# Kernel tuning notes

Hardware: AMD Instinct MI355X
Metric: run time of the kernel (lower is better)

## Reference

```python
import jax, jax.numpy as jnp
import numpy as np

N, D, K_FRAC = 4096, 256, 0.5
EPS = 1e-5  # BatchNorm1d default eps


def setup_inputs() -> dict:
    key = jax.random.key(0)
    kg, kh, kw = jax.random.split(key, 3)
    # sparse binary adjacency with self-loops so all degrees > 0 (pow(D,-1) finite)
    g = (jax.random.uniform(kg, (N, N)) < 0.004).astype(jnp.float32)
    g = jnp.maximum(g, jnp.eye(N, dtype=jnp.float32))
    h = jax.random.normal(kh, (N, D), dtype=jnp.float32)
    return {
        "g": g,
        "h": h,
        "gamma": jnp.ones((D,), jnp.float32),
        "beta": jnp.zeros((D,), jnp.float32),
        "w_proj": jax.random.normal(kw, (D, 1), dtype=jnp.float32) / np.sqrt(D),
        "b_proj": jnp.zeros((1,), jnp.float32),
        "sigma1": jnp.array([0.2], jnp.float32),
    }


def reference(g, h, gamma, beta, w_proj, b_proj, sigma1):
    # BatchNorm1d in training mode: batch statistics over the node axis
    mu = h.mean(0)
    var = h.var(0)  # biased variance, as torch uses for normalization
    h = (h - mu) / jnp.sqrt(var + EPS) * gamma + beta

    deg = g.sum(1)                               # [N] == Z2
    agg = (g @ h) / deg[:, None]                 # diag(D^-1) @ (g @ h), no NxN diag materialized
    Z1 = jnp.abs(h - agg).sum(1)                 # [N]
    pl = jax.nn.sigmoid(Z1 + deg)
    Z3 = (agg @ w_proj + b_proj)[:, 0]           # proj(Z3).squeeze()
    pg = jax.nn.softmax(Z3)                      # 1-D softmax (dim 0)
    pt = jax.nn.sigmoid(pl + pg)
    pf = jax.nn.sigmoid((h @ w_proj + b_proj)[:, 0])
    scores = sigma1[0] * pt + (1.0 - sigma1[0]) * pf

    # top_k_graph
    k = max(2, int(K_FRAC * N))
    _, idx = jax.lax.top_k(scores, k)            # [k]
    h_att = scores[:, None] * h                  # score-weighted features
    un_g = (g != 0).astype(jnp.float32)
    two_hop = ((un_g @ un_g) != 0).astype(jnp.float32)  # binarized 2-hop adjacency
    a_hat = two_hop[idx, :]                      # [k, N] row gather
    new_h = a_hat @ h_att                        # [k, D]
    g_new = a_hat[:, idx]                        # [k, k] column gather
    # norm_g: torch broadcast divides COLUMN j by row-sum degrees[j]
    g_new = g_new / g_new.sum(1)
    return g_new, new_h, idx
```

## Files before the change

### kernel.cpp

```cpp
#include <hip/hip_runtime.h>
#include <math.h>

#define NN 4096
#define DD 256
#define KK 2048
#define NW 64

__global__ void k_stats_part(const float* __restrict__ h, double* __restrict__ psum,
                             double* __restrict__ psq) {
    int d = threadIdx.x;
    int b = blockIdx.x;
    int r0 = b * 64;
    double s0=0,s1=0,s2=0,s3=0,q0=0,q1=0,q2=0,q3=0;
    for (int k = 0; k < 64; k += 4) {
        double x0 = (double)h[(size_t)(r0+k+0) * DD + d];
        double x1 = (double)h[(size_t)(r0+k+1) * DD + d];
        double x2 = (double)h[(size_t)(r0+k+2) * DD + d];
        double x3 = (double)h[(size_t)(r0+k+3) * DD + d];
        s0 += x0; q0 += x0*x0;
        s1 += x1; q1 += x1*x1;
        s2 += x2; q2 += x2*x2;
        s3 += x3; q3 += x3*x3;
    }
    psum[b * DD + d] = (s0+s1)+(s2+s3);
    psq [b * DD + d] = (q0+q1)+(q2+q3);
}

__global__ void k_stats_final(const double* __restrict__ psum, const double* __restrict__ psq,
                              double* __restrict__ mu, double* __restrict__ rstd) {
    __shared__ double rs[4][DD];
    __shared__ double rq[4][DD];
    int t = threadIdx.x;
    int d = t & (DD - 1);
    int q = t >> 8;
    double s0=0,s1=0,q0=0,q1=0;
    int b0 = q * 16;
    for (int k = 0; k < 16; k += 2) {
        s0 += psum[(b0+k)   * DD + d];
        s1 += psum[(b0+k+1) * DD + d];
        q0 += psq [(b0+k)   * DD + d];
        q1 += psq [(b0+k+1) * DD + d];
    }
    rs[q][d] = s0 + s1;
    rq[q][d] = q0 + q1;
    __syncthreads();
    if (q == 0) {
        double S  = (rs[0][d]+rs[1][d]) + (rs[2][d]+rs[3][d]);
        double Q  = (rq[0][d]+rq[1][d]) + (rq[2][d]+rq[3][d]);
        double m  = S / (double)NN;
        double var = Q / (double)NN - m * m;
        mu[d]   = m;
        rstd[d] = 1.0 / sqrt(var + 1e-5);
    }
}

__global__ void k_norm_zpf(const float* __restrict__ h, const double* __restrict__ mu,
                           const double* __restrict__ rstd, const float* __restrict__ gamma,
                           const float* __restrict__ beta, const float* __restrict__ w,
                           const float* __restrict__ bp, float* __restrict__ hn,
                           double* __restrict__ zpf) {
    __shared__ double red[DD];
    int r = blockIdx.x;
    int d = threadIdx.x;
    size_t i = (size_t)r * DD + d;
    double hnd = ((double)h[i] - mu[d]) * rstd[d] * (double)gamma[d] + (double)beta[d];
    hn[i] = (float)hnd;
    red[d] = hnd * (double)w[d];
    __syncthreads();
    for (int s = 128; s > 0; s >>= 1) {
        if (d < s) red[d] += red[d + s];
        __syncthreads();
    }
    if (d == 0) zpf[r] = red[0] + (double)bp[0];
}

__global__ void k_bitmask(const float* __restrict__ g, unsigned long long* __restrict__ B) {
    int i = blockIdx.x;
    int t = threadIdx.x;
    int q = t >> 6, l = t & 63;
    const float4* g4 = (const float4*)(g + (size_t)i * NN);
    for (int wi = 0; wi < 4; ++wi) {
        float4 v = g4[q * 256 + wi * 64 + l];
        unsigned int nib = (unsigned int)(v.x != 0.f)
                         | ((unsigned int)(v.y != 0.f) << 1)
                         | ((unsigned int)(v.z != 0.f) << 2)
                         | ((unsigned int)(v.w != 0.f) << 3);
        unsigned long long word = (unsigned long long)nib << (4 * (l & 15));
        unsigned int lo = (unsigned int)word, hi = (unsigned int)(word >> 32);
        for (int s = 1; s < 16; s <<= 1) {
            lo |= __shfl_xor(lo, s, 16);
            hi |= __shfl_xor(hi, s, 16);
        }
        if ((l & 15) == 0)
            B[(size_t)i * NW + 16 * q + 4 * wi + (l >> 4)] =
                ((unsigned long long)hi << 32) | lo;
    }
}

__global__ void k_twohop(const unsigned long long* __restrict__ B,
                         unsigned long long* __restrict__ T) {
    int i = blockIdx.x;
    int t = threadIdx.x;
    int w = t >> 6, l = t & 63;
    __shared__ int cols[128];
    __shared__ int s_cnt;
    __shared__ unsigned long long red[4][NW];
    if (t < 64) {
        unsigned long long word = B[(size_t)i * NW + t];
        int pc = __popcll(word);
        int off = pc;
        for (int dlt = 1; dlt < 64; dlt <<= 1) {
            int n = __shfl_up(off, dlt);
            if (t >= dlt) off += n;
        }
        if (t == 63) s_cnt = off;
        int base = off - pc;
        while (word) {
            int b = (int)__ffsll(word) - 1;
            word &= word - 1;
            if (base < 128) cols[base] = t * 64 + b;
            ++base;
        }
    }
    __syncthreads();
    int cnt = s_cnt;
    unsigned long long a0 = 0ull, a1 = 0ull;
    int j = w;
    for (; j + 4 < cnt; j += 8) {
        a0 |= B[(size_t)cols[j]     * NW + l];
        a1 |= B[(size_t)cols[j + 4] * NW + l];
    }
    for (; j < cnt; j += 4) a0 |= B[(size_t)cols[j] * NW + l];
    red[w][l] = a0 | a1;
    __syncthreads();
    if (t < NW)
        T[(size_t)i * NW + t] = (red[0][t] | red[1][t]) | (red[2][t] | red[3][t]);
}

__global__ void k_agg(const float* __restrict__ h, const double* __restrict__ mu,
                      const double* __restrict__ rstd, const float* __restrict__ gamma,
                      const float* __restrict__ beta, const unsigned long long* __restrict__ B,
                      const float* __restrict__ w, const float* __restrict__ bp,
                      double* __restrict__ Z1, double* __restrict__ Z3,
                      int* __restrict__ degi) {
    int i = blockIdx.x;
    int t = threadIdx.x;
    int wv = t >> 6, l = t & 63;
    __shared__ int cols[128];
    __shared__ int s_cnt;
    __shared__ double redd[4][DD];
    __shared__ double red[DD];
    __shared__ double red2[DD];
    if (t < 64) {
        unsigned long long word = B[(size_t)i * NW + t];
        int pc = __popcll(word);
        int off = pc;
        for (int dlt = 1; dlt < 64; dlt <<= 1) {
            int n = __shfl_up(off, dlt);
            if (t >= dlt) off += n;
        }
        if (t == 63) s_cnt = off;
        int base = off - pc;
        while (word) {
            int b = (int)__ffsll(word) - 1;
            word &= word - 1;
            if (base < 128) cols[base] = t * 64 + b;
            ++base;
        }
    }
    __syncthreads();
    int cnt = s_cnt;
    if (t == 0) degi[i] = cnt;
    const float4* h4 = (const float4*)h;
    double a0=0,a1=0,a2=0,a3=0,b0=0,b1=0,b2=0,b3=0;
    int j = wv;
    for (; j + 4 < cnt; j += 8) {
        float4 v0 = h4[(size_t)cols[j]     * 64 + l];
        float4 v1 = h4[(size_t)cols[j + 4] * 64 + l];
        a0 += (double)v0.x; a1 += (double)v0.y; a2 += (double)v0.z; a3 += (double)v0.w;
        b0 += (double)v1.x; b1 += (double)v1.y; b2 += (double)v1.z; b3 += (double)v1.w;
    }
    for (; j < cnt; j += 4) {
        float4 v0 = h4[(size_t)cols[j] * 64 + l];
        a0 += (double)v0.x; a1 += (double)v0.y; a2 += (double)v0.z; a3 += (double)v0.w;
    }
    redd[wv][4*l+0] = a0 + b0;
    redd[wv][4*l+1] = a1 + b1;
    redd[wv][4*l+2] = a2 + b2;
    redd[wv][4*l+3] = a3 + b3;
    __syncthreads();
    double S = (redd[0][t] + redd[1][t]) + (redd[2][t] + redd[3][t]);
    double mud = mu[t], rsd = rstd[t];
    double aggd = (S / (double)cnt - mud) * rsd * (double)gamma[t] + (double)beta[t];
    double hni  = ((double)h[(size_t)i * DD + t] - mud) * rsd * (double)gamma[t] + (double)beta[t];
    red[t]  = fabs(hni - aggd);
    red2[t] = aggd * (double)w[t];
    __syncthreads();
    for (int s = 128; s > 0; s >>= 1) {
        if (t < s) { red[t] += red[t + s]; red2[t] += red2[t + s]; }
        __syncthreads();
    }
    if (t == 0) { Z1[i] = red[0]; Z3[i] = red2[0] + (double)bp[0]; }
}

__global__ void k_red1(const double* __restrict__ Z3, double* __restrict__ pm,
                       double* __restrict__ ps, unsigned long long* __restrict__ S) {
    __shared__ double sm[128];
    __shared__ double ss[128];
    int t = threadIdx.x;
    int b = blockIdx.x;
    if (b == 0 && t < NW) S[t] = 0ull;
    double z = Z3[b * 128 + t];
    sm[t] = z;
    __syncthreads();
    for (int s = 64; s > 0; s >>= 1) {
        if (t < s) sm[t] = fmax(sm[t], sm[t + s]);
        __syncthreads();
    }
    double m = sm[0];
    ss[t] = exp(z - m);
    __syncthreads();
    for (int s = 64; s > 0; s >>= 1) {
        if (t < s) ss[t] += ss[t + s];
        __syncthreads();
    }
    if (t == 0) { pm[b] = m; ps[b] = ss[0]; }
}

__global__ void k_scorekeys(const double* __restrict__ Z1, const double* __restrict__ Z3,
                            const double* __restrict__ zpf, const int* __restrict__ degi,
                            const float* __restrict__ sigma1, const double* __restrict__ pm,
                            const double* __restrict__ ps, float* __restrict__ scores,
                            unsigned long long* __restrict__ keys) {
    int i = blockIdx.x * 256 + threadIdx.x;
    double M = -1e300;
    for (int b = 0; b < 32; ++b) M = fmax(M, pm[b]);
    double sum = 0.0;
    for (int b = 0; b < 32; ++b) sum += ps[b] * exp(pm[b] - M);
    double s1 = (double)sigma1[0];
    double pg = exp(Z3[i] - M) / sum;
    double pl = 1.0 / (1.0 + exp(-(Z1[i] + (double)degi[i])));
    double pt = 1.0 / (1.0 + exp(-(pl + pg)));
    double pf = 1.0 / (1.0 + exp(-zpf[i]));
    float sc = (float)(s1 * pt + (1.0 - s1) * pf);
    scores[i] = sc;
    unsigned int b2 = __float_as_uint(sc);
    unsigned int ka = (b2 & 0x80000000u) ? ~b2 : (b2 ^ 0x80000000u);
    keys[i] = ((unsigned long long)(~ka) << 32) | (unsigned int)i;
}

__global__ void k_rank(const unsigned long long* __restrict__ keys, int* __restrict__ idx_int,
                       unsigned long long* __restrict__ S, float* __restrict__ out_idx) {
    __shared__ unsigned long long Kl[NN];
    int t = threadIdx.x;
    for (int i = t; i < NN; i += 256) Kl[i] = keys[i];
    __syncthreads();
    int il = t >> 4, sub = t & 15;
    int i = blockIdx.x * 16 + il;
    unsigned long long ki = Kl[i];
    int c0 = 0, c1 = 0, c2 = 0, c3 = 0;
    for (int jj = 0; jj < 256; jj += 4) {
        int j = sub + (jj << 4);
        c0 += (Kl[j]      < ki) ? 1 : 0;
        c1 += (Kl[j + 16] < ki) ? 1 : 0;
        c2 += (Kl[j + 32] < ki) ? 1 : 0;
        c3 += (Kl[j + 48] < ki) ? 1 : 0;
    }
    int cnt = (c0 + c1) + (c2 + c3);
    for (int off = 8; off > 0; off >>= 1) cnt += __shfl_down(cnt, off, 16);
    if (sub == 0) {
        int rank = cnt;
        if (rank < KK) {
            idx_int[rank] = i;
            out_idx[rank] = (float)i;
            atomicOr(&S[i >> 6], 1ull << (i & 63));
        }
    }
}

__global__ void k_rowsum(const unsigned long long* __restrict__ T, const int* __restrict__ idx_int,
                         const unsigned long long* __restrict__ S, float* __restrict__ inv_rs) {
    int j = blockIdx.x * 256 + threadIdx.x;
    if (j >= KK) return;
    int r = idx_int[j];
    int c = 0;
    for (int w = 0; w < NW; ++w) c += __popcll(T[(size_t)r * NW + w] & S[w]);
    inv_rs[j] = 1.0f / (float)c;
}

__global__ void k_gnew(const unsigned long long* __restrict__ T, const int* __restrict__ idx_int,
                       const float* __restrict__ inv_rs, float* __restrict__ out) {
    int r = blockIdx.x;
    int t = threadIdx.x;
    __shared__ unsigned long long Tl[NW];
    if (t < NW) Tl[t] = T[(size_t)idx_int[r] * NW + t];
    __syncthreads();
    const int4*   idx4 = (const int4*)idx_int;
    const float4* irs4 = (const float4*)inv_rs;
    float4* out4 = (float4*)(out + (size_t)r * KK);
    for (int c4 = t; c4 < KK / 4; c4 += 256) {
        int4 jc = idx4[c4];
        float4 iv = irs4[c4];
        float4 o;
        o.x = ((Tl[jc.x >> 6] >> (jc.x & 63)) & 1ull) ? iv.x : 0.0f;
        o.y = ((Tl[jc.y >> 6] >> (jc.y & 63)) & 1ull) ? iv.y : 0.0f;
        o.z = ((Tl[jc.z >> 6] >> (jc.z & 63)) & 1ull) ? iv.z : 0.0f;
        o.w = ((Tl[jc.w >> 6] >> (jc.w & 63)) & 1ull) ? iv.w : 0.0f;
        out4[c4] = o;
    }
}

__global__ void k_newh(const unsigned long long* __restrict__ T, const int* __restrict__ idx_int,
                       const float* __restrict__ scores, const float* __restrict__ hn,
                       float* __restrict__ out) {
    int r = blockIdx.x;
    int t = threadIdx.x;
    int wv = t >> 6, l = t & 63;
    __shared__ int cols[2048];
    __shared__ int s_cnt;
    __shared__ float4 red[4][64];
    if (t < 64) {
        unsigned long long word = T[(size_t)idx_int[r] * NW + t];
        int pc = __popcll(word);
        int off = pc;
        for (int dlt = 1; dlt < 64; dlt <<= 1) {
            int n = __shfl_up(off, dlt);
            if (t >= dlt) off += n;
        }
        if (t == 63) s_cnt = off;
        int base = off - pc;
        while (word) {
            int b = (int)__ffsll(word) - 1;
            word &= word - 1;
            if (base < 2048) cols[base] = t * 64 + b;
            ++base;
        }
    }
    __syncthreads();
    int cnt = s_cnt < 2048 ? s_cnt : 2048;
    const float4* hn4 = (const float4*)hn;
    float4 a0 = {0,0,0,0}, a1 = {0,0,0,0};
    int j = wv;
    for (; j + 4 < cnt; j += 8) {
        int c0 = cols[j], c1 = cols[j + 4];
        float s0 = scores[c0], s1 = scores[c1];
        float4 v0 = hn4[(size_t)c0 * 64 + l];
        float4 v1 = hn4[(size_t)c1 * 64 + l];
        a0.x = fmaf(s0, v0.x, a0.x); a0.y = fmaf(s0, v0.y, a0.y);
        a0.z = fmaf(s0, v0.z, a0.z); a0.w = fmaf(s0, v0.w, a0.w);
        a1.x = fmaf(s1, v1.x, a1.x); a1.y = fmaf(s1, v1.y, a1.y);
        a1.z = fmaf(s1, v1.z, a1.z); a1.w = fmaf(s1, v1.w, a1.w);
    }
    for (; j < cnt; j += 4) {
        int c0 = cols[j];
        float s0 = scores[c0];
        float4 v0 = hn4[(size_t)c0 * 64 + l];
        a0.x = fmaf(s0, v0.x, a0.x); a0.y = fmaf(s0, v0.y, a0.y);
        a0.z = fmaf(s0, v0.z, a0.z); a0.w = fmaf(s0, v0.w, a0.w);
    }
    float4 acc;
    acc.x = a0.x + a1.x; acc.y = a0.y + a1.y; acc.z = a0.z + a1.z; acc.w = a0.w + a1.w;
    red[wv][l] = acc;
    __syncthreads();
    if (t < 64) {
        float4 r0 = red[0][t], r1 = red[1][t], r2 = red[2][t], r3 = red[3][t];
        float4 o;
        o.x = (r0.x + r1.x) + (r2.x + r3.x);
        o.y = (r0.y + r1.y) + (r2.y + r3.y);
        o.z = (r0.z + r1.z) + (r2.z + r3.z);
        o.w = (r0.w + r1.w) + (r2.w + r3.w);
        ((float4*)(out + (size_t)r * DD))[t] = o;
    }
}

extern "C" void kernel_launch(void* const* d_in, const int* in_sizes, int n_in,
                              void* d_out, int out_size, void* d_ws, size_t ws_size,
                              hipStream_t stream) {
    const float* g      = (const float*)d_in[0];
    const float* h      = (const float*)d_in[1];
    const float* gamma  = (const float*)d_in[2];
    const float* beta   = (const float*)d_in[3];
    const float* w_proj = (const float*)d_in[4];
    const float* b_proj = (const float*)d_in[5];
    const float* sigma1 = (const float*)d_in[6];

    char* p = (char*)d_ws;
    auto alloc = [&](size_t bytes) -> void* {
        void* q = (void*)p;
        p += (bytes + 255) & ~(size_t)255;
        return q;
    };
    double* mu      = (double*)alloc(DD * 8);
    double* rstd    = (double*)alloc(DD * 8);
    double* psum    = (double*)alloc(64 * DD * 8);
    double* psq     = (double*)alloc(64 * DD * 8);
    double* zpf     = (double*)alloc(NN * 8);
    double* Z1      = (double*)alloc(NN * 8);
    double* Z3      = (double*)alloc(NN * 8);
    double* pm      = (double*)alloc(32 * 8);
    double* ps      = (double*)alloc(32 * 8);
    int*    degi    = (int*)alloc(NN * 4);
    float*  scores  = (float*)alloc(NN * 4);
    unsigned long long* keys = (unsigned long long*)alloc(NN * 8);
    int*    idx_int = (int*)alloc(KK * 4);
    unsigned long long* S = (unsigned long long*)alloc(NW * 8);
    float*  inv_rs  = (float*)alloc(KK * 4);
    unsigned long long* B = (unsigned long long*)alloc((size_t)NN * NW * 8);
    unsigned long long* T = (unsigned long long*)alloc((size_t)NN * NW * 8);
    float*  hn      = (float*)alloc((size_t)NN * DD * 4);

    float* out_gnew = (float*)d_out;
    float* out_newh = out_gnew + (size_t)KK * KK;
    float* out_idx  = out_newh + (size_t)KK * DD;

    hipLaunchKernelGGL(k_stats_part,  dim3(64),  dim3(256),  0, stream, h, psum, psq);
    hipLaunchKernelGGL(k_stats_final, dim3(1),   dim3(1024), 0, stream, psum, psq, mu, rstd);
    hipLaunchKernelGGL(k_norm_zpf,    dim3(NN),  dim3(256),  0, stream, h, mu, rstd, gamma, beta, w_proj, b_proj, hn, zpf);
    hipLaunchKernelGGL(k_bitmask,     dim3(NN),  dim3(256),  0, stream, g, B);
    hipLaunchKernelGGL(k_twohop,      dim3(NN),  dim3(256),  0, stream, B, T);
    hipLaunchKernelGGL(k_agg,         dim3(NN),  dim3(256),  0, stream, h, mu, rstd, gamma, beta, B, w_proj, b_proj, Z1, Z3, degi);
    hipLaunchKernelGGL(k_red1,        dim3(32),  dim3(128),  0, stream, Z3, pm, ps, S);
    hipLaunchKernelGGL(k_scorekeys,   dim3(16),  dim3(256),  0, stream, Z1, Z3, zpf, degi, sigma1, pm, ps, scores, keys);
    hipLaunchKernelGGL(k_rank,        dim3(256), dim3(256),  0, stream, keys, idx_int, S, out_idx);
    hipLaunchKernelGGL(k_rowsum,      dim3(8),   dim3(256),  0, stream, T, idx_int, S, inv_rs);
    hipLaunchKernelGGL(k_gnew,        dim3(KK),  dim3(256),  0, stream, T, idx_int, inv_rs, out_gnew);
    hipLaunchKernelGGL(k_newh,        dim3(KK),  dim3(256),  0, stream, T, idx_int, scores, hn, out_newh);
}
```

Before: 202.2 us.

## Merge independent kernels into combined launches and use one wave per row

Several independent kernels are merged into shared launches that branch on block index: stats with bitmask, normalize with two-hop, and g_new with new_h. The softmax partial reduction is folded into the score kernel, and the selection bitset S is dropped. The two-hop and aggregation kernels now process one row per wavefront, using wave shuffles in place of shared-memory block reductions. This cuts launch count and synchronization overhead, but each wave now walks its neighbor list serially and score blocks redundantly recompute the global softmax reductions.

```diff
diff --git a/kernel.cpp b/kernel.cpp
--- a/kernel.cpp
+++ b/kernel.cpp
@@ -6,24 +6,68 @@
 #define KK 2048
 #define NW 64
 
-__global__ void k_stats_part(const float* __restrict__ h, double* __restrict__ psum,
-                             double* __restrict__ psq) {
-    int d = threadIdx.x;
-    int b = blockIdx.x;
-    int r0 = b * 64;
-    double s0=0,s1=0,s2=0,s3=0,q0=0,q1=0,q2=0,q3=0;
-    for (int k = 0; k < 64; k += 4) {
-        double x0 = (double)h[(size_t)(r0+k+0) * DD + d];
-        double x1 = (double)h[(size_t)(r0+k+1) * DD + d];
-        double x2 = (double)h[(size_t)(r0+k+2) * DD + d];
-        double x3 = (double)h[(size_t)(r0+k+3) * DD + d];
-        s0 += x0; q0 += x0*x0;
-        s1 += x1; q1 += x1*x1;
-        s2 += x2; q2 += x2*x2;
-        s3 += x3; q3 += x3*x3;
-    }
-    psum[b * DD + d] = (s0+s1)+(s2+s3);
-    psq [b * DD + d] = (q0+q1)+(q2+q3);
+__device__ __forceinline__ int build_list(const unsigned long long* __restrict__ B, int r,
+                                          int l, int* cols, int cap) {
+    unsigned long long word = B[(size_t)r * NW + l];
+    int pc = __popcll(word);
+    int off = pc;
+    for (int d = 1; d < 64; d <<= 1) {
+        int n = __shfl_up(off, d);
+        if (l >= d) off += n;
+    }
+    int total = __shfl(off, 63);
+    int base = off - pc;
+    while (word) {
+        int b = (int)__ffsll(word) - 1;
+        word &= word - 1;
+        if (base < cap) cols[base] = l * 64 + b;
+        ++base;
+    }
+    return total;
+}
+
+__global__ void k_pre(const float* __restrict__ h, const float* __restrict__ g,
+                      double* __restrict__ psum, double* __restrict__ psq,
+                      unsigned long long* __restrict__ B) {
+    int blk = blockIdx.x;
+    int t = threadIdx.x;
+    if (blk < 64) {
+        int d = t;
+        int r0 = blk * 64;
+        double s0=0,s1=0,s2=0,s3=0,q0=0,q1=0,q2=0,q3=0;
+        for (int k = 0; k < 64; k += 4) {
+            double x0 = (double)h[(size_t)(r0+k+0) * DD + d];
+            double x1 = (double)h[(size_t)(r0+k+1) * DD + d];
+            double x2 = (double)h[(size_t)(r0+k+2) * DD + d];
+            double x3 = (double)h[(size_t)(r0+k+3) * DD + d];
+            s0 += x0; q0 += x0*x0;
+            s1 += x1; q1 += x1*x1;
+            s2 += x2; q2 += x2*x2;
+            s3 += x3; q3 += x3*x3;
+        }
+        psum[blk * DD + d] = (s0+s1)+(s2+s3);
+        psq [blk * DD + d] = (q0+q1)+(q2+q3);
+    } else {
+        int i = blk - 64;
+        int q = t >> 6, l = t & 63;
+        const float4* g4 = (const float4*)(g + (size_t)i * NN);
+        for (int wi = 0; wi < 4; ++wi) {
+            float4 v = g4[q * 256 + wi * 64 + l];
+            unsigned int nib = (unsigned int)(v.x != 0.f)
+                             | ((unsigned int)(v.y != 0.f) << 1)
+                             | ((unsigned int)(v.z != 0.f) << 2)
+                             | ((unsigned int)(v.w != 0.f) << 3);
+            unsigned long long word = (unsigned long long)nib << (4 * (l & 15));
+            unsigned int lo = (unsigned int)word, hi = (unsigned int)(word >> 32);
+            for (int s = 1; s < 16; s <<= 1) {
+                lo |= __shfl_xor(lo, s, 16);
+                hi |= __shfl_xor(hi, s, 16);
+            }
+            if ((l & 15) == 0)
+                B[(size_t)i * NW + 16 * q + 4 * wi + (l >> 4)] =
+                    ((unsigned long long)hi << 32) | lo;
+        }
+    }
 }
 
 __global__ void k_stats_final(const double* __restrict__ psum, const double* __restrict__ psq,
@@ -54,189 +98,133 @@
     }
 }
 
-__global__ void k_norm_zpf(const float* __restrict__ h, const double* __restrict__ mu,
-                           const double* __restrict__ rstd, const float* __restrict__ gamma,
-                           const float* __restrict__ beta, const float* __restrict__ w,
-                           const float* __restrict__ bp, float* __restrict__ hn,
-                           double* __restrict__ zpf) {
-    __shared__ double red[DD];
-    int r = blockIdx.x;
-    int d = threadIdx.x;
-    size_t i = (size_t)r * DD + d;
-    double hnd = ((double)h[i] - mu[d]) * rstd[d] * (double)gamma[d] + (double)beta[d];
-    hn[i] = (float)hnd;
-    red[d] = hnd * (double)w[d];
-    __syncthreads();
-    for (int s = 128; s > 0; s >>= 1) {
-        if (d < s) red[d] += red[d + s];
-        __syncthreads();
-    }
-    if (d == 0) zpf[r] = red[0] + (double)bp[0];
-}
-
-__global__ void k_bitmask(const float* __restrict__ g, unsigned long long* __restrict__ B) {
-    int i = blockIdx.x;
-    int t = threadIdx.x;
-    int q = t >> 6, l = t & 63;
-    const float4* g4 = (const float4*)(g + (size_t)i * NN);
-    for (int wi = 0; wi < 4; ++wi) {
-        float4 v = g4[q * 256 + wi * 64 + l];
-        unsigned int nib = (unsigned int)(v.x != 0.f)
-                         | ((unsigned int)(v.y != 0.f) << 1)
-                         | ((unsigned int)(v.z != 0.f) << 2)
-                         | ((unsigned int)(v.w != 0.f) << 3);
-        unsigned long long word = (unsigned long long)nib << (4 * (l & 15));
-        unsigned int lo = (unsigned int)word, hi = (unsigned int)(word >> 32);
-        for (int s = 1; s < 16; s <<= 1) {
-            lo |= __shfl_xor(lo, s, 16);
-            hi |= __shfl_xor(hi, s, 16);
-        }
-        if ((l & 15) == 0)
-            B[(size_t)i * NW + 16 * q + 4 * wi + (l >> 4)] =
-                ((unsigned long long)hi << 32) | lo;
-    }
-}
-
-__global__ void k_twohop(const unsigned long long* __restrict__ B,
-                         unsigned long long* __restrict__ T) {
-    int i = blockIdx.x;
-    int t = threadIdx.x;
-    int w = t >> 6, l = t & 63;
-    __shared__ int cols[128];
-    __shared__ int s_cnt;
-    __shared__ unsigned long long red[4][NW];
-    if (t < 64) {
-        unsigned long long word = B[(size_t)i * NW + t];
-        int pc = __popcll(word);
-        int off = pc;
-        for (int dlt = 1; dlt < 64; dlt <<= 1) {
-            int n = __shfl_up(off, dlt);
-            if (t >= dlt) off += n;
-        }
-        if (t == 63) s_cnt = off;
-        int base = off - pc;
-        while (word) {
-            int b = (int)__ffsll(word) - 1;
-            word &= word - 1;
-            if (base < 128) cols[base] = t * 64 + b;
-            ++base;
-        }
-    }
-    __syncthreads();
-    int cnt = s_cnt;
-    unsigned long long a0 = 0ull, a1 = 0ull;
-    int j = w;
-    for (; j + 4 < cnt; j += 8) {
-        a0 |= B[(size_t)cols[j]     * NW + l];
-        a1 |= B[(size_t)cols[j + 4] * NW + l];
-    }
-    for (; j < cnt; j += 4) a0 |= B[(size_t)cols[j] * NW + l];
-    red[w][l] = a0 | a1;
-    __syncthreads();
-    if (t < NW)
-        T[(size_t)i * NW + t] = (red[0][t] | red[1][t]) | (red[2][t] | red[3][t]);
+__global__ void k_mid(const float* __restrict__ h, const double* __restrict__ mu,
+                      const double* __restrict__ rstd, const float* __restrict__ gamma,
+                      const float* __restrict__ beta, const float* __restrict__ w,
+                      const float* __restrict__ bp, float* __restrict__ hn,
+                      double* __restrict__ zpf, const unsigned long long* __restrict__ Bm,
+                      unsigned long long* __restrict__ T) {
+    __shared__ int cols[4][136];
+    int blk = blockIdx.x;
+    int t = threadIdx.x;
+    int wv = t >> 6, l = t & 63;
+    if (blk < 1024) {
+        int r = blk * 4 + wv;
+        const float4*  h4  = (const float4*)h;
+        const double2* mu2 = (const double2*)mu;
+        const double2* rs2 = (const double2*)rstd;
+        const float4*  ga4 = (const float4*)gamma;
+        const float4*  be4 = (const float4*)beta;
+        const float4*  w4  = (const float4*)w;
+        float4 hv = h4[(size_t)r * 64 + l];
+        double2 mA = mu2[2*l], mB = mu2[2*l+1];
+        double2 rA = rs2[2*l], rB = rs2[2*l+1];
+        float4 ga = ga4[l], be = be4[l], wl = w4[l];
+        double h0 = ((double)hv.x - mA.x) * rA.x * (double)ga.x + (double)be.x;
+        double h1 = ((double)hv.y - mA.y) * rA.y * (double)ga.y + (double)be.y;
+        double h2 = ((double)hv.z - mB.x) * rB.x * (double)ga.z + (double)be.z;
+        double h3 = ((double)hv.w - mB.y) * rB.y * (double)ga.w + (double)be.w;
+        float4 o = { (float)h0, (float)h1, (float)h2, (float)h3 };
+        ((float4*)hn)[(size_t)r * 64 + l] = o;
+        double acc = (h0 * (double)wl.x + h1 * (double)wl.y)
+                   + (h2 * (double)wl.z + h3 * (double)wl.w);
+        for (int off = 32; off > 0; off >>= 1) acc += __shfl_down(acc, off);
+        if (l == 0) zpf[r] = acc + (double)bp[0];
+    } else {
+        int r = (blk - 1024) * 4 + wv;
+        int cnt = build_list(Bm, r, l, cols[wv], 128);
+        if (cnt > 128) cnt = 128;
+        unsigned long long a0 = 0ull, a1 = 0ull;
+        int j = 0;
+        for (; j + 1 < cnt; j += 2) {
+            a0 |= Bm[(size_t)cols[wv][j]     * NW + l];
+            a1 |= Bm[(size_t)cols[wv][j + 1] * NW + l];
+        }
+        if (j < cnt) a0 |= Bm[(size_t)cols[wv][j] * NW + l];
+        T[(size_t)r * NW + l] = a0 | a1;
+    }
 }
 
 __global__ void k_agg(const float* __restrict__ h, const double* __restrict__ mu,
                       const double* __restrict__ rstd, const float* __restrict__ gamma,
-                      const float* __restrict__ beta, const unsigned long long* __restrict__ B,
+                      const float* __restrict__ beta, const unsigned long long* __restrict__ Bm,
                       const float* __restrict__ w, const float* __restrict__ bp,
                       double* __restrict__ Z1, double* __restrict__ Z3,
                       int* __restrict__ degi) {
-    int i = blockIdx.x;
+    __shared__ int cols[4][136];
     int t = threadIdx.x;
     int wv = t >> 6, l = t & 63;
-    __shared__ int cols[128];
-    __shared__ int s_cnt;
-    __shared__ double redd[4][DD];
-    __shared__ double red[DD];
-    __shared__ double red2[DD];
-    if (t < 64) {
-        unsigned long long word = B[(size_t)i * NW + t];
-        int pc = __popcll(word);
-        int off = pc;
-        for (int dlt = 1; dlt < 64; dlt <<= 1) {
-            int n = __shfl_up(off, dlt);
-            if (t >= dlt) off += n;
-        }
-        if (t == 63) s_cnt = off;
-        int base = off - pc;
-        while (word) {
-            int b = (int)__ffsll(word) - 1;
-            word &= word - 1;
-            if (base < 128) cols[base] = t * 64 + b;
-            ++base;
-        }
-    }
-    __syncthreads();
-    int cnt = s_cnt;
-    if (t == 0) degi[i] = cnt;
+    int r = blockIdx.x * 4 + wv;
+    int cnt = build_list(Bm, r, l, cols[wv], 128);
+    if (cnt > 128) cnt = 128;
     const float4* h4 = (const float4*)h;
-    double a0=0,a1=0,a2=0,a3=0,b0=0,b1=0,b2=0,b3=0;
-    int j = wv;
-    for (; j + 4 < cnt; j += 8) {
-        float4 v0 = h4[(size_t)cols[j]     * 64 + l];
-        float4 v1 = h4[(size_t)cols[j + 4] * 64 + l];
-        a0 += (double)v0.x; a1 += (double)v0.y; a2 += (double)v0.z; a3 += (double)v0.w;
-        b0 += (double)v1.x; b1 += (double)v1.y; b2 += (double)v1.z; b3 += (double)v1.w;
-    }
-    for (; j < cnt; j += 4) {
-        float4 v0 = h4[(size_t)cols[j] * 64 + l];
-        a0 += (double)v0.x; a1 += (double)v0.y; a2 += (double)v0.z; a3 += (double)v0.w;
-    }
-    redd[wv][4*l+0] = a0 + b0;
-    redd[wv][4*l+1] = a1 + b1;
-    redd[wv][4*l+2] = a2 + b2;
-    redd[wv][4*l+3] = a3 + b3;
-    __syncthreads();
-    double S = (redd[0][t] + redd[1][t]) + (redd[2][t] + redd[3][t]);
-    double mud = mu[t], rsd = rstd[t];
-    double aggd = (S / (double)cnt - mud) * rsd * (double)gamma[t] + (double)beta[t];
-    double hni  = ((double)h[(size_t)i * DD + t] - mud) * rsd * (double)gamma[t] + (double)beta[t];
-    red[t]  = fabs(hni - aggd);
-    red2[t] = aggd * (double)w[t];
+    double s0=0,s1=0,s2=0,s3=0,u0=0,u1=0,u2=0,u3=0;
+    int j = 0;
+    for (; j + 1 < cnt; j += 2) {
+        float4 v0 = h4[(size_t)cols[wv][j]     * 64 + l];
+        float4 v1 = h4[(size_t)cols[wv][j + 1] * 64 + l];
+        s0 += (double)v0.x; s1 += (double)v0.y; s2 += (double)v0.z; s3 += (double)v0.w;
+        u0 += (double)v1.x; u1 += (double)v1.y; u2 += (double)v1.z; u3 += (double)v1.w;
+    }
+    if (j < cnt) {
+        float4 v0 = h4[(size_t)cols[wv][j] * 64 + l];
+        s0 += (double)v0.x; s1 += (double)v0.y; s2 += (double)v0.z; s3 += (double)v0.w;
+    }
+    s0 += u0; s1 += u1; s2 += u2; s3 += u3;
+    const double2* mu2 = (const double2*)mu;
+    const double2* rs2 = (const double2*)rstd;
+    const float4*  ga4 = (const float4*)gamma;
+    const float4*  be4 = (const float4*)beta;
+    const float4*  w4  = (const float4*)w;
+    double2 mA = mu2[2*l], mB = mu2[2*l+1];
+    double2 rA = rs2[2*l], rB = rs2[2*l+1];
+    float4 ga = ga4[l], be = be4[l], wl = w4[l];
+    double inv = 1.0 / (double)cnt;
+    double g0 = (s0 * inv - mA.x) * rA.x * (double)ga.x + (double)be.x;
+    double g1 = (s1 * inv - mA.y) * rA.y * (double)ga.y + (double)be.y;
+    double g2 = (s2 * inv - mB.x) * rB.x * (double)ga.z + (double)be.z;
+    double g3 = (s3 * inv - mB.y) * rB.y * (double)ga.w + (double)be.w;
+    float4 hv = h4[(size_t)r * 64 + l];
+    double h0 = ((double)hv.x - mA.x) * rA.x * (double)ga.x + (double)be.x;
+    double h1 = ((double)hv.y - mA.y) * rA.y * (double)ga.y + (double)be.y;
+    double h2 = ((double)hv.z - mB.x) * rB.x * (double)ga.z + (double)be.z;
+    double h3 = ((double)hv.w - mB.y) * rB.y * (double)ga.w + (double)be.w;
+    double z1p = (fabs(h0 - g0) + fabs(h1 - g1)) + (fabs(h2 - g2) + fabs(h3 - g3));
+    double z3p = (g0 * (double)wl.x + g1 * (double)wl.y)
+               + (g2 * (double)wl.z + g3 * (double)wl.w);
+    for (int off = 32; off > 0; off >>= 1) {
+        z1p += __shfl_down(z1p, off);
+        z3p += __shfl_down(z3p, off);
+    }
+    if (l == 0) { Z1[r] = z1p; Z3[r] = z3p + (double)bp[0]; degi[r] = cnt; }
+}
+
+__global__ void k_scorekeys(const double* __restrict__ Z1, const double* __restrict__ Z3,
+                            const double* __restrict__ zpf, const int* __restrict__ degi,
+                            const float* __restrict__ sigma1, float* __restrict__ scores,
+                            unsigned long long* __restrict__ keys) {
+    __shared__ double red[256];
+    int t = threadIdx.x;
+    double mx = -1e300;
+    for (int k = 0; k < 16; ++k) mx = fmax(mx, Z3[t + 256 * k]);
+    red[t] = mx;
     __syncthreads();
     for (int s = 128; s > 0; s >>= 1) {
-        if (t < s) { red[t] += red[t + s]; red2[t] += red2[t + s]; }
+        if (t < s) red[t] = fmax(red[t], red[t + s]);
         __syncthreads();
     }
-    if (t == 0) { Z1[i] = red[0]; Z3[i] = red2[0] + (double)bp[0]; }
-}
-
-__global__ void k_red1(const double* __restrict__ Z3, double* __restrict__ pm,
-                       double* __restrict__ ps, unsigned long long* __restrict__ S) {
-    __shared__ double sm[128];
-    __shared__ double ss[128];
-    int t = threadIdx.x;
-    int b = blockIdx.x;
-    if (b == 0 && t < NW) S[t] = 0ull;
-    double z = Z3[b * 128 + t];
-    sm[t] = z;
+    double M = red[0];
     __syncthreads();
-    for (int s = 64; s > 0; s >>= 1) {
-        if (t < s) sm[t] = fmax(sm[t], sm[t + s]);
+    double se = 0.0;
+    for (int k = 0; k < 16; ++k) se += exp(Z3[t + 256 * k] - M);
+    red[t] = se;
+    __syncthreads();
+    for (int s = 128; s > 0; s >>= 1) {
+        if (t < s) red[t] += red[t + s];
         __syncthreads();
     }
-    double m = sm[0];
-    ss[t] = exp(z - m);
-    __syncthreads();
-    for (int s = 64; s > 0; s >>= 1) {
-        if (t < s) ss[t] += ss[t + s];
-        __syncthreads();
-    }
-    if (t == 0) { pm[b] = m; ps[b] = ss[0]; }
-}
-
-__global__ void k_scorekeys(const double* __restrict__ Z1, const double* __restrict__ Z3,
-                            const double* __restrict__ zpf, const int* __restrict__ degi,
-                            const float* __restrict__ sigma1, const double* __restrict__ pm,
-                            const double* __restrict__ ps, float* __restrict__ scores,
-                            unsigned long long* __restrict__ keys) {
-    int i = blockIdx.x * 256 + threadIdx.x;
-    double M = -1e300;
-    for (int b = 0; b < 32; ++b) M = fmax(M, pm[b]);
-    double sum = 0.0;
-    for (int b = 0; b < 32; ++b) sum += ps[b] * exp(pm[b] - M);
+    double sum = red[0];
+    int i = blockIdx.x * 256 + t;
     double s1 = (double)sigma1[0];
     double pg = exp(Z3[i] - M) / sum;
     double pl = 1.0 / (1.0 + exp(-(Z1[i] + (double)degi[i])));
@@ -250,7 +238,7 @@
 }
 
 __global__ void k_rank(const unsigned long long* __restrict__ keys, int* __restrict__ idx_int,
-                       unsigned long long* __restrict__ S, float* __restrict__ out_idx) {
+                       float* __restrict__ out_idx) {
     __shared__ unsigned long long Kl[NN];
     int t = threadIdx.x;
     for (int i = t; i < NN; i += 256) Kl[i] = keys[i];
@@ -268,108 +256,104 @@
     }
     int cnt = (c0 + c1) + (c2 + c3);
     for (int off = 8; off > 0; off >>= 1) cnt += __shfl_down(cnt, off, 16);
-    if (sub == 0) {
-        int rank = cnt;
-        if (rank < KK) {
-            idx_int[rank] = i;
-            out_idx[rank] = (float)i;
-            atomicOr(&S[i >> 6], 1ull << (i & 63));
-        }
+    if (sub == 0 && cnt < KK) {
+        idx_int[cnt] = i;
+        out_idx[cnt] = (float)i;
     }
 }
 
 __global__ void k_rowsum(const unsigned long long* __restrict__ T, const int* __restrict__ idx_int,
-                         const unsigned long long* __restrict__ S, float* __restrict__ inv_rs) {
-    int j = blockIdx.x * 256 + threadIdx.x;
-    if (j >= KK) return;
+                         float* __restrict__ inv_rs) {
+    __shared__ unsigned long long Sl[NW];
+    int t = threadIdx.x;
+    Sl[t] = 0ull;
+    for (int j = t; j < KK; j += 64) {
+        int ii = idx_int[j];
+        atomicOr(&Sl[ii >> 6], 1ull << (ii & 63));
+    }
+    int j = blockIdx.x * 64 + t;
     int r = idx_int[j];
-    int c = 0;
-    for (int w = 0; w < NW; ++w) c += __popcll(T[(size_t)r * NW + w] & S[w]);
-    inv_rs[j] = 1.0f / (float)c;
-}
-
-__global__ void k_gnew(const unsigned long long* __restrict__ T, const int* __restrict__ idx_int,
-                       const float* __restrict__ inv_rs, float* __restrict__ out) {
-    int r = blockIdx.x;
-    int t = threadIdx.x;
+    const unsigned long long* Tr = T + (size_t)r * NW;
+    int c0 = 0, c1 = 0, c2 = 0, c3 = 0;
+    for (int w = 0; w < NW; w += 4) {
+        c0 += __popcll(Tr[w]     & Sl[w]);
+        c1 += __popcll(Tr[w + 1] & Sl[w + 1]);
+        c2 += __popcll(Tr[w + 2] & Sl[w + 2]);
+        c3 += __popcll(Tr[w + 3] & Sl[w + 3]);
+    }
+    inv_rs[j] = 1.0f / (float)((c0 + c1) + (c2 + c3));
+}
+
+__global__ void k_out(const unsigned long long* __restrict__ T, const int* __restrict__ idx_int,
+                      const float* __restrict__ inv_rs, const float* __restrict__ scores,
+                      const float* __restrict__ hn, float* __restrict__ out_gnew,
+                      float* __restrict__ out_newh) {
     __shared__ unsigned long long Tl[NW];
-    if (t < NW) Tl[t] = T[(size_t)idx_int[r] * NW + t];
-    __syncthreads();
-    const int4*   idx4 = (const int4*)idx_int;
-    const float4* irs4 = (const float4*)inv_rs;
-    float4* out4 = (float4*)(out + (size_t)r * KK);
-    for (int c4 = t; c4 < KK / 4; c4 += 256) {
-        int4 jc = idx4[c4];
-        float4 iv = irs4[c4];
-        float4 o;
-        o.x = ((Tl[jc.x >> 6] >> (jc.x & 63)) & 1ull) ? iv.x : 0.0f;
-        o.y = ((Tl[jc.y >> 6] >> (jc.y & 63)) & 1ull) ? iv.y : 0.0f;
-        o.z = ((Tl[jc.z >> 6] >> (jc.z & 63)) & 1ull) ? iv.z : 0.0f;
-        o.w = ((Tl[jc.w >> 6] >> (jc.w & 63)) & 1ull) ? iv.w : 0.0f;
-        out4[c4] = o;
-    }
-}
-
-__global__ void k_newh(const unsigned long long* __restrict__ T, const int* __restrict__ idx_int,
-                       const float* __restrict__ scores, const float* __restrict__ hn,
-                       float* __restrict__ out) {
-    int r = blockIdx.x;
-    int t = threadIdx.x;
-    int wv = t >> 6, l = t & 63;
     __shared__ int cols[2048];
     __shared__ int s_cnt;
     __shared__ float4 red[4][64];
-    if (t < 64) {
-        unsigned long long word = T[(size_t)idx_int[r] * NW + t];
-        int pc = __popcll(word);
-        int off = pc;
-        for (int dlt = 1; dlt < 64; dlt <<= 1) {
-            int n = __shfl_up(off, dlt);
-            if (t >= dlt) off += n;
-        }
-        if (t == 63) s_cnt = off;
-        int base = off - pc;
-        while (word) {
-            int b = (int)__ffsll(word) - 1;
-            word &= word - 1;
-            if (base < 2048) cols[base] = t * 64 + b;
-            ++base;
-        }
-    }
-    __syncthreads();
-    int cnt = s_cnt < 2048 ? s_cnt : 2048;
-    const float4* hn4 = (const float4*)hn;
-    float4 a0 = {0,0,0,0}, a1 = {0,0,0,0};
-    int j = wv;
-    for (; j + 4 < cnt; j += 8) {
-        int c0 = cols[j], c1 = cols[j + 4];
-        float s0 = scores[c0], s1 = scores[c1];
-        float4 v0 = hn4[(size_t)c0 * 64 + l];
-        float4 v1 = hn4[(size_t)c1 * 64 + l];
-        a0.x = fmaf(s0, v0.x, a0.x); a0.y = fmaf(s0, v0.y, a0.y);
-        a0.z = fmaf(s0, v0.z, a0.z); a0.w = fmaf(s0, v0.w, a0.w);
-        a1.x = fmaf(s1, v1.x, a1.x); a1.y = fmaf(s1, v1.y, a1.y);
-        a1.z = fmaf(s1, v1.z, a1.z); a1.w = fmaf(s1, v1.w, a1.w);
-    }
-    for (; j < cnt; j += 4) {
-        int c0 = cols[j];
-        float s0 = scores[c0];
-        float4 v0 = hn4[(size_t)c0 * 64 + l];
-        a0.x = fmaf(s0, v0.x, a0.x); a0.y = fmaf(s0, v0.y, a0.y);
-        a0.z = fmaf(s0, v0.z, a0.z); a0.w = fmaf(s0, v0.w, a0.w);
-    }
-    float4 acc;
-    acc.x = a0.x + a1.x; acc.y = a0.y + a1.y; acc.z = a0.z + a1.z; acc.w = a0.w + a1.w;
-    red[wv][l] = acc;
-    __syncthreads();
-    if (t < 64) {
-        float4 r0 = red[0][t], r1 = red[1][t], r2 = red[2][t], r3 = red[3][t];
-        float4 o;
-        o.x = (r0.x + r1.x) + (r2.x + r3.x);
-        o.y = (r0.y + r1.y) + (r2.y + r3.y);
-        o.z = (r0.z + r1.z) + (r2.z + r3.z);
-        o.w = (r0.w + r1.w) + (r2.w + r3.w);
-        ((float4*)(out + (size_t)r * DD))[t] = o;
+    int blk = blockIdx.x;
+    int t = threadIdx.x;
+    if (blk < KK) {
+        int r = blk;
+        if (t < NW) Tl[t] = T[(size_t)idx_int[r] * NW + t];
+        __syncthreads();
+        const int4*   idx4 = (const int4*)idx_int;
+        const float4* irs4 = (const float4*)inv_rs;
+        float4* out4 = (float4*)(out_gnew + (size_t)r * KK);
+        for (int c4 = t; c4 < KK / 4; c4 += 256) {
+            int4 jc = idx4[c4];
+            float4 iv = irs4[c4];
+            float4 o;
+            o.x = ((Tl[jc.x >> 6] >> (jc.x & 63)) & 1ull) ? iv.x : 0.0f;
+            o.y = ((Tl[jc.y >> 6] >> (jc.y & 63)) & 1ull) ? iv.y : 0.0f;
+            o.z = ((Tl[jc.z >> 6] >> (jc.z & 63)) & 1ull) ? iv.z : 0.0f;
+            o.w = ((Tl[jc.w >> 6] >> (jc.w & 63)) & 1ull) ? iv.w : 0.0f;
+            out4[c4] = o;
+        }
+    } else {
+        int r = blk - KK;
+        int wv = t >> 6, l = t & 63;
+        if (t < 64) {
+            int total = build_list(T, idx_int[r], t, cols, 2048);
+            if (t == 63) s_cnt = total;
+        }
+        __syncthreads();
+        int cnt = s_cnt < 2048 ? s_cnt : 2048;
+        const float4* hn4 = (const float4*)hn;
+        float4 a0 = {0,0,0,0}, a1 = {0,0,0,0};
+        int j = wv;
+        for (; j + 4 < cnt; j += 8) {
+            int c0 = cols[j], c1 = cols[j + 4];
+            float s0 = scores[c0], s1 = scores[c1];
+            float4 v0 = hn4[(size_t)c0 * 64 + l];
+            float4 v1 = hn4[(size_t)c1 * 64 + l];
+            a0.x = fmaf(s0, v0.x, a0.x); a0.y = fmaf(s0, v0.y, a0.y);
+            a0.z = fmaf(s0, v0.z, a0.z); a0.w = fmaf(s0, v0.w, a0.w);
+            a1.x = fmaf(s1, v1.x, a1.x); a1.y = fmaf(s1, v1.y, a1.y);
+            a1.z = fmaf(s1, v1.z, a1.z); a1.w = fmaf(s1, v1.w, a1.w);
+        }
+        for (; j < cnt; j += 4) {
+            int c0 = cols[j];
+            float s0 = scores[c0];
+            float4 v0 = hn4[(size_t)c0 * 64 + l];
+            a0.x = fmaf(s0, v0.x, a0.x); a0.y = fmaf(s0, v0.y, a0.y);
+            a0.z = fmaf(s0, v0.z, a0.z); a0.w = fmaf(s0, v0.w, a0.w);
+        }
+        float4 acc;
+        acc.x = a0.x + a1.x; acc.y = a0.y + a1.y;
+        acc.z = a0.z + a1.z; acc.w = a0.w + a1.w;
+        red[wv][l] = acc;
+        __syncthreads();
+        if (t < 64) {
+            float4 r0 = red[0][t], r1 = red[1][t], r2 = red[2][t], r3 = red[3][t];
+            float4 o;
+            o.x = (r0.x + r1.x) + (r2.x + r3.x);
+            o.y = (r0.y + r1.y) + (r2.y + r3.y);
+            o.z = (r0.z + r1.z) + (r2.z + r3.z);
+            o.w = (r0.w + r1.w) + (r2.w + r3.w);
+            ((float4*)(out_newh + (size_t)r * DD))[t] = o;
+        }
     }
 }
 
@@ -397,13 +381,10 @@
     double* zpf     = (double*)alloc(NN * 8);
     double* Z1      = (double*)alloc(NN * 8);
     double* Z3      = (double*)alloc(NN * 8);
-    double* pm      = (double*)alloc(32 * 8);
-    double* ps      = (double*)alloc(32 * 8);
     int*    degi    = (int*)alloc(NN * 4);
     float*  scores  = (float*)alloc(NN * 4);
     unsigned long long* keys = (unsigned long long*)alloc(NN * 8);
     int*    idx_int = (int*)alloc(KK * 4);
-    unsigned long long* S = (unsigned long long*)alloc(NW * 8);
     float*  inv_rs  = (float*)alloc(KK * 4);
     unsigned long long* B = (unsigned long long*)alloc((size_t)NN * NW * 8);
     unsigned long long* T = (unsigned long long*)alloc((size_t)NN * NW * 8);
@@ -413,16 +394,12 @@
     float* out_newh = out_gnew + (size_t)KK * KK;
     float* out_idx  = out_newh + (size_t)KK * DD;
 
-    hipLaunchKernelGGL(k_stats_part,  dim3(64),  dim3(256),  0, stream, h, psum, psq);
-    hipLaunchKernelGGL(k_stats_final, dim3(1),   dim3(1024), 0, stream, psum, psq, mu, rstd);
-    hipLaunchKernelGGL(k_norm_zpf,    dim3(NN),  dim3(256),  0, stream, h, mu, rstd, gamma, beta, w_proj, b_proj, hn, zpf);
-    hipLaunchKernelGGL(k_bitmask,     dim3(NN),  dim3(256),  0, stream, g, B);
-    hipLaunchKernelGGL(k_twohop,      dim3(NN),  dim3(256),  0, stream, B, T);
-    hipLaunchKernelGGL(k_agg,         dim3(NN),  dim3(256),  0, stream, h, mu, rstd, gamma, beta, B, w_proj, b_proj, Z1, Z3, degi);
-    hipLaunchKernelGGL(k_red1,        dim3(32),  dim3(128),  0, stream, Z3, pm, ps, S);
-    hipLaunchKernelGGL(k_scorekeys,   dim3(16),  dim3(256),  0, stream, Z1, Z3, zpf, degi, sigma1, pm, ps, scores, keys);
-    hipLaunchKernelGGL(k_rank,        dim3(256), dim3(256),  0, stream, keys, idx_int, S, out_idx);
-    hipLaunchKernelGGL(k_rowsum,      dim3(8),   dim3(256),  0, stream, T, idx_int, S, inv_rs);
-    hipLaunchKernelGGL(k_gnew,        dim3(KK),  dim3(256),  0, stream, T, idx_int, inv_rs, out_gnew);
-    hipLaunchKernelGGL(k_newh,        dim3(KK),  dim3(256),  0, stream, T, idx_int, scores, hn, out_newh);
-}
+    hipLaunchKernelGGL(k_pre,         dim3(64 + NN), dim3(256),  0, stream, h, g, psum, psq, B);
+    hipLaunchKernelGGL(k_stats_final, dim3(1),       dim3(1024), 0, stream, psum, psq, mu, rstd);
+    hipLaunchKernelGGL(k_mid,         dim3(2048),    dim3(256),  0, stream, h, mu, rstd, gamma, beta, w_proj, b_proj, hn, zpf, B, T);
+    hipLaunchKernelGGL(k_agg,         dim3(1024),    dim3(256),  0, stream, h, mu, rstd, gamma, beta, B, w_proj, b_proj, Z1, Z3, degi);
+    hipLaunchKernelGGL(k_scorekeys,   dim3(16),      dim3(256),  0, stream, Z1, Z3, zpf, degi, sigma1, scores, keys);
+    hipLaunchKernelGGL(k_rank,        dim3(256),     dim3(256),  0, stream, keys, idx_int, out_idx);
+    hipLaunchKernelGGL(k_rowsum,      dim3(32),      dim3(64),   0, stream, T, idx_int, inv_rs);
+    hipLaunchKernelGGL(k_out,         dim3(2 * KK),  dim3(256),  0, stream, T, idx_int, inv_rs, scores, hn, out_gnew, out_newh);
+}
```

Result: faster. 185.4 us (-8.3%).
